# Kernel optimization log

Hardware: AMD Instinct MI355X
Metric: run time of the kernel (lower is better)

The kernel has to match this reference:

```python
import jax, jax.numpy as jnp
import numpy as np

DENSE_W = 0.7  # unused in learned fusion path but kept for parity
SPARSE_W = 0.3

def _l2norm(x):
    return x / jnp.linalg.norm(x, axis=-1, keepdims=True)

def setup_inputs() -> dict:
    key = jax.random.key(0)
    ks = jax.random.split(key, 8)
    Q, D, dim = 32, 4096, 384
    feat = 2 * dim + 2  # 770
    query_dense = _l2norm(jax.random.normal(ks[0], (Q, dim), jnp.float32))
    doc_dense = _l2norm(jax.random.normal(ks[1], (D, dim), jnp.float32))
    sparse_scores = jax.random.uniform(ks[2], (Q, D), jnp.float32)
    W1 = jax.random.normal(ks[3], (feat, 384), jnp.float32) * (1.0 / np.sqrt(feat))
    b1 = jnp.zeros((384,), jnp.float32)
    W2 = jax.random.normal(ks[4], (384, 192), jnp.float32) * (1.0 / np.sqrt(384))
    b2 = jnp.zeros((192,), jnp.float32)
    W3 = jax.random.normal(ks[5], (192, 1), jnp.float32) * (1.0 / np.sqrt(192))
    b3 = jnp.zeros((1,), jnp.float32)
    return {"query_dense": query_dense, "doc_dense": doc_dense,
            "sparse_scores": sparse_scores,
            "W1": W1, "b1": b1, "W2": W2, "b2": b2, "W3": W3, "b3": b3}

def reference(query_dense, doc_dense, sparse_scores, W1, b1, W2, b2, W3, b3):
    # dense cosine similarity (inputs are L2-normalized): [Q, D]
    dense_scores = query_dense @ doc_dense.T
    Q, D = dense_scores.shape
    dim = query_dense.shape[1]
    # Vectorized equivalent of the per-pair gather+concat double loop:
    # feature[q, d] = [query_dense[q], doc_dense[d], dense[q,d], sparse[q,d]]
    qf = jnp.broadcast_to(query_dense[:, None, :], (Q, D, dim))
    df = jnp.broadcast_to(doc_dense[None, :, :], (Q, D, dim))
    features = jnp.concatenate(
        [qf, df, dense_scores[..., None], sparse_scores[..., None]], axis=-1)  # [Q, D, 2*dim+2]
    # 4-layer fusion MLP (Dropout is identity at inference)
    h = jax.nn.relu(features @ W1 + b1)
    h = jax.nn.relu(h @ W2 + b2)
    fusion_weights = jax.nn.sigmoid((h @ W3 + b3)[..., 0])  # [Q, D]
    final_scores = fusion_weights * dense_scores + (1.0 - fusion_weights) * sparse_scores
    return final_scores, dense_scores, sparse_scores
```

## Files before the change

### kernel.cpp

```cpp
#include <hip/hip_runtime.h>
#include <hip/hip_bf16.h>

typedef __attribute__((ext_vector_type(4)))  float f32x4;
typedef __attribute__((ext_vector_type(16))) float f32x16;
typedef __attribute__((ext_vector_type(8)))  short bf16x8;
typedef __attribute__((ext_vector_type(4)))  unsigned int u32x4;

__device__ __forceinline__ short f2bf(float x){
    __hip_bfloat16 h = __float2bfloat16(x);
    return __builtin_bit_cast(short, h);
}
__device__ __forceinline__ float bf2f(short x){
    unsigned int u = ((unsigned int)(unsigned short)x) << 16;
    return __builtin_bit_cast(float, u);
}
__device__ __forceinline__ unsigned int pk2bf(float x, float y){
    union { __hip_bfloat162 h; unsigned int u; } cv;
    float2 f; f.x = x; f.y = y;
    cv.h = __float22bfloat162_rn(f);
    return cv.u;
}

__global__ __launch_bounds__(256)
void pre_kernel(const float* __restrict__ query, const float* __restrict__ doc,
                const float* __restrict__ sparse, const float* __restrict__ W1,
                const float* __restrict__ b1,
                float* __restrict__ out_dense, float* __restrict__ out_sparse,
                short* __restrict__ Bws, float* __restrict__ Aq){
    __shared__ float ldsq[32*388];
    __shared__ float ldsd[16*388];
    const int b = blockIdx.x, tid = threadIdx.x;

    if (b < 256){
        const int d0 = b*16;
        #pragma unroll
        for (int i=0;i<12;i++){ int idx = tid + i*256; int row = idx/96, c4 = idx%96;
            *(f32x4*)(ldsq + row*388 + c4*4) = *(const f32x4*)(query + row*384 + c4*4); }
        #pragma unroll
        for (int i=0;i<6;i++){ int idx = tid + i*256; int row = idx/96, c4 = idx%96;
            *(f32x4*)(ldsd + row*388 + c4*4) = *(const f32x4*)(doc + (d0+row)*384 + c4*4); }
        __syncthreads();
        const int q = tid>>3, dg = tid&7;
        float acc0 = 0.0f, acc1 = 0.0f;
        #pragma unroll 4
        for (int k=0;k<384;k++){
            float qv = ldsq[q*388 + k];
            acc0 += qv*ldsd[dg*388 + k];
            acc1 += qv*ldsd[(dg+8)*388 + k];
        }
        out_dense[q*4096 + d0 + dg]     = acc0;
        out_dense[q*4096 + d0 + dg + 8] = acc1;
        if (tid < 128){
            int qq = tid>>2, c4 = tid&3;
            *(f32x4*)(out_sparse + qq*4096 + d0 + c4*4) = *(const f32x4*)(sparse + qq*4096 + d0 + c4*4);
        }
    } else {
        const int bb = b - 256;
        const int w = tid >> 6, lane = tid & 63;
        const int cl = lane & 15, quad = lane >> 4;
        const float* src; const float* wrow; int r0; bool isA;
        if (bb < 256){ r0 = bb*16;       src = doc;   wrow = W1 + 384*384; isA = false; }
        else         { r0 = (bb-256)*16; src = query; wrow = W1;           isA = true;  }

        f32x4 acc[6];
        #pragma unroll
        for (int t=0;t<6;t++) acc[t] = (f32x4){0.f,0.f,0.f,0.f};

        #pragma unroll 1
        for (int s=0;s<12;s++){
            const float* ap = src + (r0+cl)*384 + s*32 + quad*8;
            const f32x4 a0 = *(const f32x4*)ap;
            const f32x4 a1 = *(const f32x4*)(ap+4);
            u32x4 afu;
            afu[0] = pk2bf(a0[0], a0[1]); afu[1] = pk2bf(a0[2], a0[3]);
            afu[2] = pk2bf(a1[0], a1[1]); afu[3] = pk2bf(a1[2], a1[3]);
            const bf16x8 af = __builtin_bit_cast(bf16x8, afu);
            const float* wk = wrow + (s*32 + quad*8)*384;
            #pragma unroll
            for (int tt=0;tt<6;tt++){
                const int col = (w*6+tt)*16 + cl;
                u32x4 bu;
                #pragma unroll
                for (int p=0;p<4;p++)
                    bu[p] = pk2bf(wk[(2*p)*384 + col], wk[(2*p+1)*384 + col]);
                const bf16x8 bf_ = __builtin_bit_cast(bf16x8, bu);
                acc[tt] = __builtin_amdgcn_mfma_f32_16x16x32_bf16(af, bf_, acc[tt], 0, 0, 0);
            }
        }
        #pragma unroll
        for (int tt=0;tt<6;tt++){
            const int col = (w*6+tt)*16 + cl;
            if (isA){
                const float b1v = b1[col];
                #pragma unroll
                for (int r=0;r<4;r++)
                    Aq[(r0 + quad*4 + r)*384 + col] = acc[tt][r] + b1v;
            } else {
                #pragma unroll
                for (int r=0;r<4;r++)
                    Bws[(r0 + quad*4 + r)*384 + col] = f2bf(acc[tt][r]);
            }
        }
    }
}

__global__ __launch_bounds__(512, 2)
void main_kernel(const float* __restrict__ Aq, const short* __restrict__ Bws,
                 const float* __restrict__ W1,
                 const float* __restrict__ b2, const float* __restrict__ W3,
                 const float* __restrict__ b3, const float* __restrict__ sparse,
                 const float* __restrict__ W2, const float* __restrict__ dense_in,
                 float* __restrict__ out_final){
    __shared__ short lw[73728];
    const int tid = threadIdx.x;
    #pragma unroll
    for (int i=0;i<18;i++){
        int c = tid + i*512;
        int lane_c = c & 63, st = c >> 6;
        int s = st/6, t2 = st%6;
        int n = t2*32 + (lane_c&31), kb = s*16 + ((lane_c>>5)&1)*8;
        u32x4 vu;
        #pragma unroll
        for (int p=0;p<4;p++)
            vu[p] = pk2bf(W2[(kb+2*p)*192 + n], W2[(kb+2*p+1)*192 + n]);
        *(bf16x8*)(lw + c*8) = __builtin_bit_cast(bf16x8, vu);
    }
    __syncthreads();

    const int lane = tid & 63, w = tid >> 6;
    const int m = lane & 31, q2 = lane >> 5;
    const int kbase = q2*8;
    const float b3v = b3[0];
    const float* w1c = W1 + 768*384;
    const float* w1d = W1 + 769*384;

    #pragma unroll 1
    for (int t4=0; t4<2; t4++){
        const int dcol = blockIdx.x*16 + t4*8 + w;
        const float dsv = dense_in[m*4096 + dcol];
        const float ssv = sparse[m*4096 + dcol];

        f32x16 acc[6];
        #pragma unroll
        for (int t=0;t<6;t++)
            #pragma unroll
            for (int r=0;r<16;r++) acc[t][r] = 0.0f;

        bf16x8 bw_c = *(const bf16x8*)(Bws + dcol*384 + kbase);
        f32x4  a0_c = *(const f32x4*)(Aq + m*384 + kbase);
        f32x4  a1_c = *(const f32x4*)(Aq + m*384 + kbase + 4);
        bf16x8 bfr_c[6];
        #pragma unroll
        for (int t=0;t<6;t++) bfr_c[t] = *(const bf16x8*)(lw + (t*64 + lane)*8);

        #pragma unroll 1
        for (int s=0;s<24;s++){
            const int k0 = s*16 + kbase;
            const int kn = (s < 23) ? (k0 + 16) : kbase;
            const int sn = (s < 23) ? (s + 1) : 0;
            const bf16x8 bw_n = *(const bf16x8*)(Bws + dcol*384 + kn);
            const f32x4  a0_n = *(const f32x4*)(Aq + m*384 + kn);
            const f32x4  a1_n = *(const f32x4*)(Aq + m*384 + kn + 4);
            bf16x8 bfr_n[6];
            #pragma unroll
            for (int t=0;t<6;t++) bfr_n[t] = *(const bf16x8*)(lw + ((sn*6 + t)*64 + lane)*8);

            const f32x4 wc0 = *(const f32x4*)(w1c + k0);
            const f32x4 wc1 = *(const f32x4*)(w1c + k0 + 4);
            const f32x4 wd0 = *(const f32x4*)(w1d + k0);
            const f32x4 wd1 = *(const f32x4*)(w1d + k0 + 4);
            float hv[8];
            #pragma unroll
            for (int j=0;j<4;j++){
                hv[j]   = fmaxf(a0_c[j] + bf2f(bw_c[j])   + dsv*wc0[j] + ssv*wd0[j], 0.0f);
                hv[4+j] = fmaxf(a1_c[j] + bf2f(bw_c[4+j]) + dsv*wc1[j] + ssv*wd1[j], 0.0f);
            }
            u32x4 fru;
            fru[0] = pk2bf(hv[0], hv[1]); fru[1] = pk2bf(hv[2], hv[3]);
            fru[2] = pk2bf(hv[4], hv[5]); fru[3] = pk2bf(hv[6], hv[7]);
            const bf16x8 fr = __builtin_bit_cast(bf16x8, fru);

            #pragma unroll
            for (int t=0;t<6;t++)
                acc[t] = __builtin_amdgcn_mfma_f32_32x32x16_bf16(fr, bfr_c[t], acc[t], 0, 0, 0);

            bw_c = bw_n; a0_c = a0_n; a1_c = a1_n;
            #pragma unroll
            for (int t=0;t<6;t++) bfr_c[t] = bfr_n[t];
        }

        float p[16];
        #pragma unroll
        for (int r=0;r<16;r++) p[r] = 0.0f;
        #pragma unroll
        for (int t=0;t<6;t++){
            const int n = t*32 + m;
            const float b2v = b2[n];
            const float w3v = W3[n];
            #pragma unroll
            for (int r=0;r<16;r++)
                p[r] += fmaxf(acc[t][r] + b2v, 0.0f) * w3v;
        }
        #pragma unroll
        for (int mask=1; mask<32; mask<<=1){
            #pragma unroll
            for (int r=0;r<16;r++) p[r] += __shfl_xor(p[r], mask);
        }
        float myp = p[0];
        #pragma unroll
        for (int r=1;r<16;r++) myp = (m==r) ? p[r] : myp;
        if (m < 16){
            const int row = (m&3) + 8*(m>>2) + 4*q2;
            float logit = myp + b3v;
            float wgt = 1.0f/(1.0f + __expf(-logit));
            float dd = dense_in[row*4096 + dcol];
            float ss = sparse[row*4096 + dcol];
            out_final[row*4096 + dcol] = wgt*dd + (1.0f - wgt)*ss;
        }
    }
}

extern "C" void kernel_launch(void* const* d_in, const int* in_sizes, int n_in,
                              void* d_out, int out_size, void* d_ws, size_t ws_size,
                              hipStream_t stream){
    const float* query  = (const float*)d_in[0];
    const float* doc    = (const float*)d_in[1];
    const float* sparse = (const float*)d_in[2];
    const float* W1     = (const float*)d_in[3];
    const float* b1     = (const float*)d_in[4];
    const float* W2     = (const float*)d_in[5];
    const float* b2     = (const float*)d_in[6];
    const float* W3     = (const float*)d_in[7];
    const float* b3     = (const float*)d_in[8];

    float* out_final  = (float*)d_out;
    float* out_dense  = (float*)d_out + 131072;
    float* out_sparse = (float*)d_out + 262144;

    short* Bws = (short*)d_ws;
    float* Aq  = (float*)((char*)d_ws + 3145728);

    hipLaunchKernelGGL(pre_kernel,  dim3(514), dim3(256), 0, stream,
                       query, doc, sparse, W1, b1, out_dense, out_sparse, Bws, Aq);
    hipLaunchKernelGGL(main_kernel, dim3(256), dim3(512), 0, stream,
                       Aq, Bws, W1, b2, W3, b3, sparse, W2, out_dense, out_final);
}
```

Before: 143.4 us.

## Split W2 columns across wave pairs, use MFMA for dense scores, fp32 Bws

The dense-score computation moves from a scalar LDS dot-product loop to bf16 MFMA on fewer blocks, and the sparse copy becomes its own set of blocks. In the main kernel, each wave now handles two doc columns but only half of the W2 output columns. Each W2 fragment read from LDS is therefore reused for two MFMAs, and the old double-buffered register copy of all six fragments is gone. Partial layer-3 sums are combined across the wave pair through shared memory, which adds two block barriers per iteration. Bws is stored as fp32 instead of bf16, which doubles that workspace traffic, and the dense scores now carry bf16 rounding error.

```diff
diff --git a/kernel.cpp b/kernel.cpp
--- a/kernel.cpp
+++ b/kernel.cpp
@@ -6,10 +6,6 @@
 typedef __attribute__((ext_vector_type(8)))  short bf16x8;
 typedef __attribute__((ext_vector_type(4)))  unsigned int u32x4;
 
-__device__ __forceinline__ short f2bf(float x){
-    __hip_bfloat16 h = __float2bfloat16(x);
-    return __builtin_bit_cast(short, h);
-}
 __device__ __forceinline__ float bf2f(short x){
     unsigned int u = ((unsigned int)(unsigned short)x) << 16;
     return __builtin_bit_cast(float, u);
@@ -20,44 +16,47 @@
     cv.h = __float22bfloat162_rn(f);
     return cv.u;
 }
+__device__ __forceinline__ bf16x8 pk8(const f32x4 lo, const f32x4 hi){
+    u32x4 u;
+    u[0] = pk2bf(lo[0], lo[1]); u[1] = pk2bf(lo[2], lo[3]);
+    u[2] = pk2bf(hi[0], hi[1]); u[3] = pk2bf(hi[2], hi[3]);
+    return __builtin_bit_cast(bf16x8, u);
+}
 
 __global__ __launch_bounds__(256)
 void pre_kernel(const float* __restrict__ query, const float* __restrict__ doc,
                 const float* __restrict__ sparse, const float* __restrict__ W1,
                 const float* __restrict__ b1,
                 float* __restrict__ out_dense, float* __restrict__ out_sparse,
-                short* __restrict__ Bws, float* __restrict__ Aq){
-    __shared__ float ldsq[32*388];
-    __shared__ float ldsd[16*388];
+                float* __restrict__ Bws, float* __restrict__ Aq){
     const int b = blockIdx.x, tid = threadIdx.x;
-
-    if (b < 256){
-        const int d0 = b*16;
-        #pragma unroll
-        for (int i=0;i<12;i++){ int idx = tid + i*256; int row = idx/96, c4 = idx%96;
-            *(f32x4*)(ldsq + row*388 + c4*4) = *(const f32x4*)(query + row*384 + c4*4); }
-        #pragma unroll
-        for (int i=0;i<6;i++){ int idx = tid + i*256; int row = idx/96, c4 = idx%96;
-            *(f32x4*)(ldsd + row*388 + c4*4) = *(const f32x4*)(doc + (d0+row)*384 + c4*4); }
-        __syncthreads();
-        const int q = tid>>3, dg = tid&7;
-        float acc0 = 0.0f, acc1 = 0.0f;
-        #pragma unroll 4
-        for (int k=0;k<384;k++){
-            float qv = ldsq[q*388 + k];
-            acc0 += qv*ldsd[dg*388 + k];
-            acc1 += qv*ldsd[(dg+8)*388 + k];
-        }
-        out_dense[q*4096 + d0 + dg]     = acc0;
-        out_dense[q*4096 + d0 + dg + 8] = acc1;
-        if (tid < 128){
-            int qq = tid>>2, c4 = tid&3;
-            *(f32x4*)(out_sparse + qq*4096 + d0 + c4*4) = *(const f32x4*)(sparse + qq*4096 + d0 + c4*4);
-        }
-    } else {
-        const int bb = b - 256;
-        const int w = tid >> 6, lane = tid & 63;
-        const int cl = lane & 15, quad = lane >> 4;
+    const int w = tid >> 6, lane = tid & 63;
+    const int cl = lane & 15, quad = lane >> 4;
+
+    if (b < 64){
+        const int dbase = b*64 + w*16;
+        f32x4 acc0 = (f32x4){0.f,0.f,0.f,0.f};
+        f32x4 acc1 = (f32x4){0.f,0.f,0.f,0.f};
+        #pragma unroll 1
+        for (int s=0;s<12;s++){
+            const int k0 = s*32 + quad*8;
+            const float* dp = doc + (dbase + cl)*384 + k0;
+            const bf16x8 af = pk8(*(const f32x4*)dp, *(const f32x4*)(dp+4));
+            const float* q0p = query + cl*384 + k0;
+            const float* q1p = query + (16+cl)*384 + k0;
+            const bf16x8 bf0 = pk8(*(const f32x4*)q0p, *(const f32x4*)(q0p+4));
+            const bf16x8 bf1 = pk8(*(const f32x4*)q1p, *(const f32x4*)(q1p+4));
+            acc0 = __builtin_amdgcn_mfma_f32_16x16x32_bf16(af, bf0, acc0, 0, 0, 0);
+            acc1 = __builtin_amdgcn_mfma_f32_16x16x32_bf16(af, bf1, acc1, 0, 0, 0);
+        }
+        #pragma unroll
+        for (int r=0;r<4;r++){
+            const int d = dbase + quad*4 + r;
+            out_dense[cl*4096 + d]      = acc0[r];
+            out_dense[(16+cl)*4096 + d] = acc1[r];
+        }
+    } else if (b < 322){
+        const int bb = b - 64;
         const float* src; const float* wrow; int r0; bool isA;
         if (bb < 256){ r0 = bb*16;       src = doc;   wrow = W1 + 384*384; isA = false; }
         else         { r0 = (bb-256)*16; src = query; wrow = W1;           isA = true;  }
@@ -69,12 +68,7 @@
         #pragma unroll 1
         for (int s=0;s<12;s++){
             const float* ap = src + (r0+cl)*384 + s*32 + quad*8;
-            const f32x4 a0 = *(const f32x4*)ap;
-            const f32x4 a1 = *(const f32x4*)(ap+4);
-            u32x4 afu;
-            afu[0] = pk2bf(a0[0], a0[1]); afu[1] = pk2bf(a0[2], a0[3]);
-            afu[2] = pk2bf(a1[0], a1[1]); afu[3] = pk2bf(a1[2], a1[3]);
-            const bf16x8 af = __builtin_bit_cast(bf16x8, afu);
+            const bf16x8 af = pk8(*(const f32x4*)ap, *(const f32x4*)(ap+4));
             const float* wk = wrow + (s*32 + quad*8)*384;
             #pragma unroll
             for (int tt=0;tt<6;tt++){
@@ -87,31 +81,34 @@
                 acc[tt] = __builtin_amdgcn_mfma_f32_16x16x32_bf16(af, bf_, acc[tt], 0, 0, 0);
             }
         }
+        float* out = isA ? Aq : Bws;
         #pragma unroll
         for (int tt=0;tt<6;tt++){
             const int col = (w*6+tt)*16 + cl;
-            if (isA){
-                const float b1v = b1[col];
-                #pragma unroll
-                for (int r=0;r<4;r++)
-                    Aq[(r0 + quad*4 + r)*384 + col] = acc[tt][r] + b1v;
-            } else {
-                #pragma unroll
-                for (int r=0;r<4;r++)
-                    Bws[(r0 + quad*4 + r)*384 + col] = f2bf(acc[tt][r]);
-            }
+            const float b1v = isA ? b1[col] : 0.0f;
+            #pragma unroll
+            for (int r=0;r<4;r++)
+                out[(r0 + quad*4 + r)*384 + col] = acc[tt][r] + b1v;
+        }
+    } else {
+        const int base = (b - 322)*1024;
+        #pragma unroll
+        for (int i=0;i<4;i++){
+            int v = base + i*256 + tid;
+            *(f32x4*)(out_sparse + v*4) = *(const f32x4*)(sparse + v*4);
         }
     }
 }
 
 __global__ __launch_bounds__(512, 2)
-void main_kernel(const float* __restrict__ Aq, const short* __restrict__ Bws,
+void main_kernel(const float* __restrict__ Aq, const float* __restrict__ Bws,
                  const float* __restrict__ W1,
                  const float* __restrict__ b2, const float* __restrict__ W3,
                  const float* __restrict__ b3, const float* __restrict__ sparse,
                  const float* __restrict__ W2, const float* __restrict__ dense_in,
                  float* __restrict__ out_final){
     __shared__ short lw[73728];
+    __shared__ float pbuf[4][2][2][32];
     const int tid = threadIdx.x;
     #pragma unroll
     for (int i=0;i<18;i++){
@@ -130,93 +127,110 @@
     const int lane = tid & 63, w = tid >> 6;
     const int m = lane & 31, q2 = lane >> 5;
     const int kbase = q2*8;
+    const int pair = w >> 1, h = w & 1;
     const float b3v = b3[0];
     const float* w1c = W1 + 768*384;
     const float* w1d = W1 + 769*384;
 
     #pragma unroll 1
     for (int t4=0; t4<2; t4++){
-        const int dcol = blockIdx.x*16 + t4*8 + w;
-        const float dsv = dense_in[m*4096 + dcol];
-        const float ssv = sparse[m*4096 + dcol];
-
-        f32x16 acc[6];
-        #pragma unroll
-        for (int t=0;t<6;t++)
-            #pragma unroll
-            for (int r=0;r<16;r++) acc[t][r] = 0.0f;
-
-        bf16x8 bw_c = *(const bf16x8*)(Bws + dcol*384 + kbase);
-        f32x4  a0_c = *(const f32x4*)(Aq + m*384 + kbase);
-        f32x4  a1_c = *(const f32x4*)(Aq + m*384 + kbase + 4);
-        bf16x8 bfr_c[6];
-        #pragma unroll
-        for (int t=0;t<6;t++) bfr_c[t] = *(const bf16x8*)(lw + (t*64 + lane)*8);
+        const int dcol0 = blockIdx.x*16 + t4*8 + pair*2;
+        const int dcol1 = dcol0 + 1;
+        const float dsv0 = dense_in[m*4096 + dcol0];
+        const float ssv0 = sparse[m*4096 + dcol0];
+        const float dsv1 = dense_in[m*4096 + dcol1];
+        const float ssv1 = sparse[m*4096 + dcol1];
+
+        f32x16 acc0[3], acc1[3];
+        #pragma unroll
+        for (int t=0;t<3;t++)
+            #pragma unroll
+            for (int r=0;r<16;r++){ acc0[t][r] = 0.0f; acc1[t][r] = 0.0f; }
+
+        f32x4 a0_c = *(const f32x4*)(Aq + m*384 + kbase);
+        f32x4 a1_c = *(const f32x4*)(Aq + m*384 + kbase + 4);
+        f32x4 b00_c = *(const f32x4*)(Bws + dcol0*384 + kbase);
+        f32x4 b01_c = *(const f32x4*)(Bws + dcol0*384 + kbase + 4);
+        f32x4 b10_c = *(const f32x4*)(Bws + dcol1*384 + kbase);
+        f32x4 b11_c = *(const f32x4*)(Bws + dcol1*384 + kbase + 4);
 
         #pragma unroll 1
         for (int s=0;s<24;s++){
             const int k0 = s*16 + kbase;
             const int kn = (s < 23) ? (k0 + 16) : kbase;
-            const int sn = (s < 23) ? (s + 1) : 0;
-            const bf16x8 bw_n = *(const bf16x8*)(Bws + dcol*384 + kn);
-            const f32x4  a0_n = *(const f32x4*)(Aq + m*384 + kn);
-            const f32x4  a1_n = *(const f32x4*)(Aq + m*384 + kn + 4);
-            bf16x8 bfr_n[6];
-            #pragma unroll
-            for (int t=0;t<6;t++) bfr_n[t] = *(const bf16x8*)(lw + ((sn*6 + t)*64 + lane)*8);
-
+            const f32x4 a0_n  = *(const f32x4*)(Aq + m*384 + kn);
+            const f32x4 a1_n  = *(const f32x4*)(Aq + m*384 + kn + 4);
+            const f32x4 b00_n = *(const f32x4*)(Bws + dcol0*384 + kn);
+            const f32x4 b01_n = *(const f32x4*)(Bws + dcol0*384 + kn + 4);
+            const f32x4 b10_n = *(const f32x4*)(Bws + dcol1*384 + kn);
+            const f32x4 b11_n = *(const f32x4*)(Bws + dcol1*384 + kn + 4);
             const f32x4 wc0 = *(const f32x4*)(w1c + k0);
             const f32x4 wc1 = *(const f32x4*)(w1c + k0 + 4);
             const f32x4 wd0 = *(const f32x4*)(w1d + k0);
             const f32x4 wd1 = *(const f32x4*)(w1d + k0 + 4);
-            float hv[8];
+
+            f32x4 h00, h01, h10, h11;
             #pragma unroll
             for (int j=0;j<4;j++){
-                hv[j]   = fmaxf(a0_c[j] + bf2f(bw_c[j])   + dsv*wc0[j] + ssv*wd0[j], 0.0f);
-                hv[4+j] = fmaxf(a1_c[j] + bf2f(bw_c[4+j]) + dsv*wc1[j] + ssv*wd1[j], 0.0f);
-            }
-            u32x4 fru;
-            fru[0] = pk2bf(hv[0], hv[1]); fru[1] = pk2bf(hv[2], hv[3]);
-            fru[2] = pk2bf(hv[4], hv[5]); fru[3] = pk2bf(hv[6], hv[7]);
-            const bf16x8 fr = __builtin_bit_cast(bf16x8, fru);
-
-            #pragma unroll
-            for (int t=0;t<6;t++)
-                acc[t] = __builtin_amdgcn_mfma_f32_32x32x16_bf16(fr, bfr_c[t], acc[t], 0, 0, 0);
-
-            bw_c = bw_n; a0_c = a0_n; a1_c = a1_n;
-            #pragma unroll
-            for (int t=0;t<6;t++) bfr_c[t] = bfr_n[t];
-        }
-
-        float p[16];
-        #pragma unroll
-        for (int r=0;r<16;r++) p[r] = 0.0f;
-        #pragma unroll
-        for (int t=0;t<6;t++){
-            const int n = t*32 + m;
+                h00[j] = fmaxf(a0_c[j] + b00_c[j] + dsv0*wc0[j] + ssv0*wd0[j], 0.0f);
+                h01[j] = fmaxf(a1_c[j] + b01_c[j] + dsv0*wc1[j] + ssv0*wd1[j], 0.0f);
+                h10[j] = fmaxf(a0_c[j] + b10_c[j] + dsv1*wc0[j] + ssv1*wd0[j], 0.0f);
+                h11[j] = fmaxf(a1_c[j] + b11_c[j] + dsv1*wc1[j] + ssv1*wd1[j], 0.0f);
+            }
+            const bf16x8 fr0 = pk8(h00, h01);
+            const bf16x8 fr1 = pk8(h10, h11);
+
+            #pragma unroll
+            for (int t=0;t<3;t++){
+                const bf16x8 bfr = *(const bf16x8*)(lw + ((s*6 + h*3 + t)*64 + lane)*8);
+                acc0[t] = __builtin_amdgcn_mfma_f32_32x32x16_bf16(fr0, bfr, acc0[t], 0, 0, 0);
+                acc1[t] = __builtin_amdgcn_mfma_f32_32x32x16_bf16(fr1, bfr, acc1[t], 0, 0, 0);
+            }
+            a0_c = a0_n; a1_c = a1_n;
+            b00_c = b00_n; b01_c = b01_n; b10_c = b10_n; b11_c = b11_n;
+        }
+
+        float p0[16], p1[16];
+        #pragma unroll
+        for (int r=0;r<16;r++){ p0[r] = 0.0f; p1[r] = 0.0f; }
+        #pragma unroll
+        for (int t=0;t<3;t++){
+            const int n = (h*3 + t)*32 + m;
             const float b2v = b2[n];
             const float w3v = W3[n];
             #pragma unroll
-            for (int r=0;r<16;r++)
-                p[r] += fmaxf(acc[t][r] + b2v, 0.0f) * w3v;
+            for (int r=0;r<16;r++){
+                p0[r] += fmaxf(acc0[t][r] + b2v, 0.0f) * w3v;
+                p1[r] += fmaxf(acc1[t][r] + b2v, 0.0f) * w3v;
+            }
         }
         #pragma unroll
         for (int mask=1; mask<32; mask<<=1){
             #pragma unroll
-            for (int r=0;r<16;r++) p[r] += __shfl_xor(p[r], mask);
-        }
-        float myp = p[0];
-        #pragma unroll
-        for (int r=1;r<16;r++) myp = (m==r) ? p[r] : myp;
+            for (int r=0;r<16;r++){ p0[r] += __shfl_xor(p0[r], mask); p1[r] += __shfl_xor(p1[r], mask); }
+        }
+        float my0 = p0[0], my1 = p1[0];
+        #pragma unroll
+        for (int r=1;r<16;r++){ my0 = (m==r) ? p0[r] : my0; my1 = (m==r) ? p1[r] : my1; }
         if (m < 16){
             const int row = (m&3) + 8*(m>>2) + 4*q2;
-            float logit = myp + b3v;
-            float wgt = 1.0f/(1.0f + __expf(-logit));
-            float dd = dense_in[row*4096 + dcol];
-            float ss = sparse[row*4096 + dcol];
-            out_final[row*4096 + dcol] = wgt*dd + (1.0f - wgt)*ss;
-        }
+            pbuf[pair][h][0][row] = my0;
+            pbuf[pair][h][1][row] = my1;
+        }
+        __syncthreads();
+        if (h == 0 && m < 16){
+            const int row = (m&3) + 8*(m>>2) + 4*q2;
+            #pragma unroll
+            for (int dc=0; dc<2; dc++){
+                const int dcol = dcol0 + dc;
+                float logit = pbuf[pair][0][dc][row] + pbuf[pair][1][dc][row] + b3v;
+                float wgt = 1.0f/(1.0f + __expf(-logit));
+                float dd = dense_in[row*4096 + dcol];
+                float ss = sparse[row*4096 + dcol];
+                out_final[row*4096 + dcol] = wgt*dd + (1.0f - wgt)*ss;
+            }
+        }
+        __syncthreads();
     }
 }
 
@@ -237,10 +251,10 @@
     float* out_dense  = (float*)d_out + 131072;
     float* out_sparse = (float*)d_out + 262144;
 
-    short* Bws = (short*)d_ws;
-    float* Aq  = (float*)((char*)d_ws + 3145728);
-
-    hipLaunchKernelGGL(pre_kernel,  dim3(514), dim3(256), 0, stream,
+    float* Bws = (float*)d_ws;
+    float* Aq  = (float*)((char*)d_ws + 6291456);
+
+    hipLaunchKernelGGL(pre_kernel,  dim3(354), dim3(256), 0, stream,
                        query, doc, sparse, W1, b1, out_dense, out_sparse, Bws, Aq);
     hipLaunchKernelGGL(main_kernel, dim3(256), dim3(512), 0, stream,
                        Aq, Bws, W1, b2, W3, b3, sparse, W2, out_dense, out_final);
```

Result: slower. 152.4 us (+6.2%).

## Fuse precompute and MLP kernels into one cooperative kernel with grid sync

Applied to the files above, without the earlier changes.

Merges the precompute kernel (dense scores, doc/query projections through W1, sparse copy) into the main MLP kernel as a single cooperative launch. Warps are split across roles before a grid-wide sync, the dense scores now use bf16 MFMA instead of scalar fp32, the doc projection is stored as fp32 instead of bf16, and the W2 register prefetch from LDS is dropped in favour of direct per-step reads. This removes one launch and the gap between kernels, at the cost of a grid barrier, more workspace traffic and lower precision in the dense scores. The dense-score output now goes through bf16 rounding, which may break tolerance.

```diff
diff --git a/kernel.cpp b/kernel.cpp
--- a/kernel.cpp
+++ b/kernel.cpp
@@ -1,118 +1,42 @@
 #include <hip/hip_runtime.h>
 #include <hip/hip_bf16.h>
+#include <hip/hip_cooperative_groups.h>
+
+namespace cg = cooperative_groups;
 
 typedef __attribute__((ext_vector_type(4)))  float f32x4;
 typedef __attribute__((ext_vector_type(16))) float f32x16;
 typedef __attribute__((ext_vector_type(8)))  short bf16x8;
 typedef __attribute__((ext_vector_type(4)))  unsigned int u32x4;
 
-__device__ __forceinline__ short f2bf(float x){
-    __hip_bfloat16 h = __float2bfloat16(x);
-    return __builtin_bit_cast(short, h);
-}
-__device__ __forceinline__ float bf2f(short x){
-    unsigned int u = ((unsigned int)(unsigned short)x) << 16;
-    return __builtin_bit_cast(float, u);
-}
 __device__ __forceinline__ unsigned int pk2bf(float x, float y){
     union { __hip_bfloat162 h; unsigned int u; } cv;
     float2 f; f.x = x; f.y = y;
     cv.h = __float22bfloat162_rn(f);
     return cv.u;
 }
-
-__global__ __launch_bounds__(256)
-void pre_kernel(const float* __restrict__ query, const float* __restrict__ doc,
-                const float* __restrict__ sparse, const float* __restrict__ W1,
-                const float* __restrict__ b1,
-                float* __restrict__ out_dense, float* __restrict__ out_sparse,
-                short* __restrict__ Bws, float* __restrict__ Aq){
-    __shared__ float ldsq[32*388];
-    __shared__ float ldsd[16*388];
-    const int b = blockIdx.x, tid = threadIdx.x;
-
-    if (b < 256){
-        const int d0 = b*16;
-        #pragma unroll
-        for (int i=0;i<12;i++){ int idx = tid + i*256; int row = idx/96, c4 = idx%96;
-            *(f32x4*)(ldsq + row*388 + c4*4) = *(const f32x4*)(query + row*384 + c4*4); }
-        #pragma unroll
-        for (int i=0;i<6;i++){ int idx = tid + i*256; int row = idx/96, c4 = idx%96;
-            *(f32x4*)(ldsd + row*388 + c4*4) = *(const f32x4*)(doc + (d0+row)*384 + c4*4); }
-        __syncthreads();
-        const int q = tid>>3, dg = tid&7;
-        float acc0 = 0.0f, acc1 = 0.0f;
-        #pragma unroll 4
-        for (int k=0;k<384;k++){
-            float qv = ldsq[q*388 + k];
-            acc0 += qv*ldsd[dg*388 + k];
-            acc1 += qv*ldsd[(dg+8)*388 + k];
-        }
-        out_dense[q*4096 + d0 + dg]     = acc0;
-        out_dense[q*4096 + d0 + dg + 8] = acc1;
-        if (tid < 128){
-            int qq = tid>>2, c4 = tid&3;
-            *(f32x4*)(out_sparse + qq*4096 + d0 + c4*4) = *(const f32x4*)(sparse + qq*4096 + d0 + c4*4);
-        }
-    } else {
-        const int bb = b - 256;
-        const int w = tid >> 6, lane = tid & 63;
-        const int cl = lane & 15, quad = lane >> 4;
-        const float* src; const float* wrow; int r0; bool isA;
-        if (bb < 256){ r0 = bb*16;       src = doc;   wrow = W1 + 384*384; isA = false; }
-        else         { r0 = (bb-256)*16; src = query; wrow = W1;           isA = true;  }
-
-        f32x4 acc[6];
-        #pragma unroll
-        for (int t=0;t<6;t++) acc[t] = (f32x4){0.f,0.f,0.f,0.f};
-
-        #pragma unroll 1
-        for (int s=0;s<12;s++){
-            const float* ap = src + (r0+cl)*384 + s*32 + quad*8;
-            const f32x4 a0 = *(const f32x4*)ap;
-            const f32x4 a1 = *(const f32x4*)(ap+4);
-            u32x4 afu;
-            afu[0] = pk2bf(a0[0], a0[1]); afu[1] = pk2bf(a0[2], a0[3]);
-            afu[2] = pk2bf(a1[0], a1[1]); afu[3] = pk2bf(a1[2], a1[3]);
-            const bf16x8 af = __builtin_bit_cast(bf16x8, afu);
-            const float* wk = wrow + (s*32 + quad*8)*384;
-            #pragma unroll
-            for (int tt=0;tt<6;tt++){
-                const int col = (w*6+tt)*16 + cl;
-                u32x4 bu;
-                #pragma unroll
-                for (int p=0;p<4;p++)
-                    bu[p] = pk2bf(wk[(2*p)*384 + col], wk[(2*p+1)*384 + col]);
-                const bf16x8 bf_ = __builtin_bit_cast(bf16x8, bu);
-                acc[tt] = __builtin_amdgcn_mfma_f32_16x16x32_bf16(af, bf_, acc[tt], 0, 0, 0);
-            }
-        }
-        #pragma unroll
-        for (int tt=0;tt<6;tt++){
-            const int col = (w*6+tt)*16 + cl;
-            if (isA){
-                const float b1v = b1[col];
-                #pragma unroll
-                for (int r=0;r<4;r++)
-                    Aq[(r0 + quad*4 + r)*384 + col] = acc[tt][r] + b1v;
-            } else {
-                #pragma unroll
-                for (int r=0;r<4;r++)
-                    Bws[(r0 + quad*4 + r)*384 + col] = f2bf(acc[tt][r]);
-            }
-        }
-    }
+__device__ __forceinline__ bf16x8 pk8(const f32x4 lo, const f32x4 hi){
+    u32x4 u;
+    u[0] = pk2bf(lo[0], lo[1]); u[1] = pk2bf(lo[2], lo[3]);
+    u[2] = pk2bf(hi[0], hi[1]); u[3] = pk2bf(hi[2], hi[3]);
+    return __builtin_bit_cast(bf16x8, u);
 }
 
 __global__ __launch_bounds__(512, 2)
-void main_kernel(const float* __restrict__ Aq, const short* __restrict__ Bws,
-                 const float* __restrict__ W1,
-                 const float* __restrict__ b2, const float* __restrict__ W3,
-                 const float* __restrict__ b3, const float* __restrict__ sparse,
-                 const float* __restrict__ W2, const float* __restrict__ dense_in,
-                 float* __restrict__ out_final){
+void fused_kernel(const float* __restrict__ query, const float* __restrict__ doc,
+                  const float* __restrict__ sparse, const float* __restrict__ W1,
+                  const float* __restrict__ b1, const float* __restrict__ W2,
+                  const float* __restrict__ b2, const float* __restrict__ W3,
+                  const float* __restrict__ b3,
+                  float* __restrict__ out_final, float* __restrict__ out_dense,
+                  float* __restrict__ out_sparse,
+                  float* __restrict__ Bws, float* __restrict__ Aq){
     __shared__ short lw[73728];
     const int tid = threadIdx.x;
+    const int lane = tid & 63, w = tid >> 6;
+    const int m = lane & 31, q2 = lane >> 5;
+    const int kbase = q2*8;
+
     #pragma unroll
     for (int i=0;i<18;i++){
         int c = tid + i*512;
@@ -125,11 +49,86 @@
             vu[p] = pk2bf(W2[(kb+2*p)*192 + n], W2[(kb+2*p+1)*192 + n]);
         *(bf16x8*)(lw + c*8) = __builtin_bit_cast(bf16x8, vu);
     }
-    __syncthreads();
-
-    const int lane = tid & 63, w = tid >> 6;
-    const int m = lane & 31, q2 = lane >> 5;
-    const int kbase = q2*8;
+
+    const int gw = blockIdx.x*8 + w;
+    if (gw < 1536){
+        const int r0 = (gw/12)*32, c0 = (gw%12)*32;
+        const float* w1b = W1 + 384*384;
+        f32x16 acc;
+        #pragma unroll
+        for (int r=0;r<16;r++) acc[r] = 0.0f;
+        #pragma unroll 1
+        for (int s=0;s<24;s++){
+            const int k0 = s*16 + kbase;
+            const float* dp = doc + (r0+m)*384 + k0;
+            const bf16x8 af = pk8(*(const f32x4*)dp, *(const f32x4*)(dp+4));
+            const float* wk = w1b + k0*384 + c0 + m;
+            u32x4 bu;
+            #pragma unroll
+            for (int p=0;p<4;p++)
+                bu[p] = pk2bf(wk[(2*p)*384], wk[(2*p+1)*384]);
+            const bf16x8 bf_ = __builtin_bit_cast(bf16x8, bu);
+            acc = __builtin_amdgcn_mfma_f32_32x32x16_bf16(af, bf_, acc, 0, 0, 0);
+        }
+        #pragma unroll
+        for (int r=0;r<16;r++){
+            const int row = (r&3) + 8*(r>>2) + 4*q2;
+            Bws[(r0+row)*384 + c0 + m] = acc[r];
+        }
+    } else if (gw < 1664){
+        const int d0 = (gw-1536)*32;
+        f32x16 acc;
+        #pragma unroll
+        for (int r=0;r<16;r++) acc[r] = 0.0f;
+        #pragma unroll 1
+        for (int s=0;s<24;s++){
+            const int k0 = s*16 + kbase;
+            const float* dp = doc + (d0+m)*384 + k0;
+            const float* qp = query + m*384 + k0;
+            const bf16x8 af = pk8(*(const f32x4*)dp, *(const f32x4*)(dp+4));
+            const bf16x8 bf_ = pk8(*(const f32x4*)qp, *(const f32x4*)(qp+4));
+            acc = __builtin_amdgcn_mfma_f32_32x32x16_bf16(af, bf_, acc, 0, 0, 0);
+        }
+        #pragma unroll
+        for (int r=0;r<16;r++){
+            const int row = (r&3) + 8*(r>>2) + 4*q2;
+            out_dense[m*4096 + d0 + row] = acc[r];
+        }
+    } else if (gw < 1676){
+        const int c0 = (gw-1664)*32;
+        f32x16 acc;
+        #pragma unroll
+        for (int r=0;r<16;r++) acc[r] = 0.0f;
+        #pragma unroll 1
+        for (int s=0;s<24;s++){
+            const int k0 = s*16 + kbase;
+            const float* qp = query + m*384 + k0;
+            const bf16x8 af = pk8(*(const f32x4*)qp, *(const f32x4*)(qp+4));
+            const float* wk = W1 + k0*384 + c0 + m;
+            u32x4 bu;
+            #pragma unroll
+            for (int p=0;p<4;p++)
+                bu[p] = pk2bf(wk[(2*p)*384], wk[(2*p+1)*384]);
+            const bf16x8 bf_ = __builtin_bit_cast(bf16x8, bu);
+            acc = __builtin_amdgcn_mfma_f32_32x32x16_bf16(af, bf_, acc, 0, 0, 0);
+        }
+        const float b1v = b1[c0 + m];
+        #pragma unroll
+        for (int r=0;r<16;r++){
+            const int row = (r&3) + 8*(r>>2) + 4*q2;
+            Aq[row*384 + c0 + m] = acc[r] + b1v;
+        }
+    } else if (gw < 1804){
+        const int base = (gw-1676)*256;
+        #pragma unroll
+        for (int i=0;i<4;i++){
+            int v = base + i*64 + lane;
+            *(f32x4*)(out_sparse + v*4) = *(const f32x4*)(sparse + v*4);
+        }
+    }
+
+    cg::this_grid().sync();
+
     const float b3v = b3[0];
     const float* w1c = W1 + 768*384;
     const float* w1d = W1 + 769*384;
@@ -137,7 +136,7 @@
     #pragma unroll 1
     for (int t4=0; t4<2; t4++){
         const int dcol = blockIdx.x*16 + t4*8 + w;
-        const float dsv = dense_in[m*4096 + dcol];
+        const float dsv = out_dense[m*4096 + dcol];
         const float ssv = sparse[m*4096 + dcol];
 
         f32x16 acc[6];
@@ -146,47 +145,36 @@
             #pragma unroll
             for (int r=0;r<16;r++) acc[t][r] = 0.0f;
 
-        bf16x8 bw_c = *(const bf16x8*)(Bws + dcol*384 + kbase);
-        f32x4  a0_c = *(const f32x4*)(Aq + m*384 + kbase);
-        f32x4  a1_c = *(const f32x4*)(Aq + m*384 + kbase + 4);
-        bf16x8 bfr_c[6];
-        #pragma unroll
-        for (int t=0;t<6;t++) bfr_c[t] = *(const bf16x8*)(lw + (t*64 + lane)*8);
+        f32x4 a0_c = *(const f32x4*)(Aq + m*384 + kbase);
+        f32x4 a1_c = *(const f32x4*)(Aq + m*384 + kbase + 4);
+        f32x4 b0_c = *(const f32x4*)(Bws + dcol*384 + kbase);
+        f32x4 b1_c = *(const f32x4*)(Bws + dcol*384 + kbase + 4);
 
         #pragma unroll 1
         for (int s=0;s<24;s++){
             const int k0 = s*16 + kbase;
             const int kn = (s < 23) ? (k0 + 16) : kbase;
-            const int sn = (s < 23) ? (s + 1) : 0;
-            const bf16x8 bw_n = *(const bf16x8*)(Bws + dcol*384 + kn);
-            const f32x4  a0_n = *(const f32x4*)(Aq + m*384 + kn);
-            const f32x4  a1_n = *(const f32x4*)(Aq + m*384 + kn + 4);
-            bf16x8 bfr_n[6];
-            #pragma unroll
-            for (int t=0;t<6;t++) bfr_n[t] = *(const bf16x8*)(lw + ((sn*6 + t)*64 + lane)*8);
-
+            const f32x4 a0_n = *(const f32x4*)(Aq + m*384 + kn);
+            const f32x4 a1_n = *(const f32x4*)(Aq + m*384 + kn + 4);
+            const f32x4 b0_n = *(const f32x4*)(Bws + dcol*384 + kn);
+            const f32x4 b1_n = *(const f32x4*)(Bws + dcol*384 + kn + 4);
             const f32x4 wc0 = *(const f32x4*)(w1c + k0);
             const f32x4 wc1 = *(const f32x4*)(w1c + k0 + 4);
             const f32x4 wd0 = *(const f32x4*)(w1d + k0);
             const f32x4 wd1 = *(const f32x4*)(w1d + k0 + 4);
-            float hv[8];
+            f32x4 h0, h1;
             #pragma unroll
             for (int j=0;j<4;j++){
-                hv[j]   = fmaxf(a0_c[j] + bf2f(bw_c[j])   + dsv*wc0[j] + ssv*wd0[j], 0.0f);
-                hv[4+j] = fmaxf(a1_c[j] + bf2f(bw_c[4+j]) + dsv*wc1[j] + ssv*wd1[j], 0.0f);
+                h0[j] = fmaxf(a0_c[j] + b0_c[j] + dsv*wc0[j] + ssv*wd0[j], 0.0f);
+                h1[j] = fmaxf(a1_c[j] + b1_c[j] + dsv*wc1[j] + ssv*wd1[j], 0.0f);
             }
-            u32x4 fru;
-            fru[0] = pk2bf(hv[0], hv[1]); fru[1] = pk2bf(hv[2], hv[3]);
-            fru[2] = pk2bf(hv[4], hv[5]); fru[3] = pk2bf(hv[6], hv[7]);
-            const bf16x8 fr = __builtin_bit_cast(bf16x8, fru);
-
-            #pragma unroll
-            for (int t=0;t<6;t++)
-                acc[t] = __builtin_amdgcn_mfma_f32_32x32x16_bf16(fr, bfr_c[t], acc[t], 0, 0, 0);
-
-            bw_c = bw_n; a0_c = a0_n; a1_c = a1_n;
-            #pragma unroll
-            for (int t=0;t<6;t++) bfr_c[t] = bfr_n[t];
+            const bf16x8 fr = pk8(h0, h1);
+            #pragma unroll
+            for (int t=0;t<6;t++){
+                const bf16x8 bfr = *(const bf16x8*)(lw + ((s*6 + t)*64 + lane)*8);
+                acc[t] = __builtin_amdgcn_mfma_f32_32x32x16_bf16(fr, bfr, acc[t], 0, 0, 0);
+            }
+            a0_c = a0_n; a1_c = a1_n; b0_c = b0_n; b1_c = b1_n;
         }
 
         float p[16];
@@ -213,7 +201,7 @@
             const int row = (m&3) + 8*(m>>2) + 4*q2;
             float logit = myp + b3v;
             float wgt = 1.0f/(1.0f + __expf(-logit));
-            float dd = dense_in[row*4096 + dcol];
+            float dd = out_dense[row*4096 + dcol];
             float ss = sparse[row*4096 + dcol];
             out_final[row*4096 + dcol] = wgt*dd + (1.0f - wgt)*ss;
         }
@@ -237,11 +225,13 @@
     float* out_dense  = (float*)d_out + 131072;
     float* out_sparse = (float*)d_out + 262144;
 
-    short* Bws = (short*)d_ws;
-    float* Aq  = (float*)((char*)d_ws + 3145728);
-
-    hipLaunchKernelGGL(pre_kernel,  dim3(514), dim3(256), 0, stream,
-                       query, doc, sparse, W1, b1, out_dense, out_sparse, Bws, Aq);
-    hipLaunchKernelGGL(main_kernel, dim3(256), dim3(512), 0, stream,
-                       Aq, Bws, W1, b2, W3, b3, sparse, W2, out_dense, out_final);
-}
+    float* Bws = (float*)d_ws;
+    float* Aq  = (float*)((char*)d_ws + 6291456);
+
+    void* args[] = { (void*)&query, (void*)&doc, (void*)&sparse, (void*)&W1, (void*)&b1,
+                     (void*)&W2, (void*)&b2, (void*)&W3, (void*)&b3,
+                     (void*)&out_final, (void*)&out_dense, (void*)&out_sparse,
+                     (void*)&Bws, (void*)&Aq };
+    hipLaunchCooperativeKernel((const void*)fused_kernel, dim3(256), dim3(512),
+                               args, 0, stream);
+}
```

Measured after the change: 193.6 us. 1.35x slower.
